# Performance work log

Hardware: AMD Instinct MI355X
Metric: run time of the kernel (lower is better)

## Reference

```python
import jax, jax.numpy as jnp
import numpy as np

NEG_INF = -(2.0**32) + 1.0  # matches tf: -2**32 + 1


def _positional_encoding(seq_len, d_model):
    # sinusoidal PE exactly as in the module (sin on even cols, cos on odd cols)
    pos = np.arange(seq_len)[:, None].astype(np.float32)
    i = np.arange(d_model)[None, :]
    angle_rates = 1.0 / np.power(10000.0, 2 * (i // 2) / np.float32(d_model))
    ang = pos * angle_rates
    ang[:, 0::2] = np.sin(ang[:, 0::2])
    ang[:, 1::2] = np.cos(ang[:, 1::2])
    return jnp.asarray(ang[None, ...], dtype=jnp.float32)  # [1, S, D]


def setup_inputs() -> dict:
    key = jax.random.key(0)
    kq, kk, kv, kw, km = jax.random.split(key, 5)
    B, S, D = 64, 512, 256
    q = jax.random.normal(kq, (B, S, D), dtype=jnp.float32)
    k = jax.random.normal(kk, (B, S, D), dtype=jnp.float32)
    v = jax.random.normal(kv, (B, S, D), dtype=jnp.float32)
    # keras 'random_uniform' initializer default range is [-0.05, 0.05]
    W = jax.random.uniform(kw, (D, D), dtype=jnp.float32, minval=-0.05, maxval=0.05)
    mask = jax.random.randint(km, (B, S), 0, 2, dtype=jnp.int32)
    return {"q": q, "k": k, "v": v, "W": W, "mask": mask}


def reference(q, k, v, W, mask):
    B, S, D = q.shape
    pe = _positional_encoding(S, D)  # [1, S, D]
    q = q + pe
    k = k + pe
    q = jax.nn.relu(jnp.einsum('bsd,de->bse', q, W))
    k = jax.nn.relu(jnp.einsum('bsd,de->bse', k, W))
    logits = jnp.einsum('bqd,bkd->bqk', q, k) / jnp.sqrt(jnp.float32(D))  # [B,S,S]
    # mask over key positions, broadcast across query dim
    logits = jnp.where(mask[:, None, :] == 0, jnp.float32(NEG_INF), logits)
    att = jax.nn.softmax(logits, axis=-1)
    out = jnp.einsum('bqk,bkd->bqd', att, v)
    return jnp.mean(out, axis=1)  # [B, D]
```

## Files before the change

kernel.cpp:

```cpp
#include <hip/hip_runtime.h>

#define NEG_INF (-4294967295.0f)

typedef _Float16 f16;
typedef _Float16 f16x8 __attribute__((ext_vector_type(8)));
typedef float f32x4 __attribute__((ext_vector_type(4)));

#define MFMA16(a,b,c) __builtin_amdgcn_mfma_f32_16x16x32_f16((a),(b),(c),0,0,0)

#if defined(__has_builtin)
#if __has_builtin(__builtin_amdgcn_global_load_lds)
#define HAS_GLD 1
#endif
#endif

__device__ __forceinline__ void stage16(const void* g, void* lds_base, int lane) {
#ifdef HAS_GLD
    __builtin_amdgcn_global_load_lds(
        (const __attribute__((address_space(1))) unsigned int*)g,
        (__attribute__((address_space(3))) unsigned int*)lds_base, 16, 0, 0);
#else
    ((f16x8*)lds_base)[lane] = *(const f16x8*)g;
#endif
}

__global__ __launch_bounds__(256) void setup_kernel(const float* __restrict__ W,
                                                    float* __restrict__ pe,
                                                    f16* __restrict__ WT,
                                                    float* __restrict__ WG,
                                                    float* __restrict__ out) {
    const int bid = blockIdx.x, t = threadIdx.x;
    if (bid < 512) {
        int idx = bid * 256 + t;
        int s = idx >> 8, d = idx & 255;
        float x = (float)(d & ~1) * (1.f / 256.f);
        float rate = exp2f(x * -13.287712379549449f);
        float ang = (float)s * rate;
        pe[idx] = (d & 1) ? cosf(ang) : sinf(ang);
    } else if (bid < 768) {
        int e = bid - 512, d = t;
        WT[(e << 8) + d] = (f16)W[(d << 8) + e];
    } else if (bid == 768) {
        #pragma unroll
        for (int i = 0; i < 128; ++i) WG[i * 256 + t] = 0.f;
    } else {
        #pragma unroll
        for (int i = 0; i < 64; ++i) out[i * 256 + t] = 0.f;
    }
}

__global__ __launch_bounds__(256, 4) void proj_kernel(const float* __restrict__ q,
                                                      const float* __restrict__ k,
                                                      const f16* __restrict__ WT,
                                                      const float* __restrict__ pe,
                                                      f16* __restrict__ outp) {
    __shared__ __align__(16) f16 Ws[256 * 64];
    const int t = threadIdx.x, l = t & 63, wv = t >> 6, lr = l & 15, lg = l >> 4;
    const int r0 = blockIdx.x * 64;
    const float* src = (r0 < 32768) ? q : k;
    const int rb = r0 & 32767;

    const float* arow = src + (size_t)(rb + wv * 16 + lr) * 256;
    const float* prow = pe + (size_t)((rb + wv * 16 + lr) & 511) * 256;
    f16x8 af[8];
    #pragma unroll
    for (int kk = 0; kk < 8; ++kk) {
        int d = kk * 32 + lg * 8;
        float4 a0 = *(const float4*)(arow + d);
        float4 a1 = *(const float4*)(arow + d + 4);
        float4 p0 = *(const float4*)(prow + d);
        float4 p1 = *(const float4*)(prow + d + 4);
        f16x8 h;
        h[0] = (f16)(a0.x + p0.x); h[1] = (f16)(a0.y + p0.y);
        h[2] = (f16)(a0.z + p0.z); h[3] = (f16)(a0.w + p0.w);
        h[4] = (f16)(a1.x + p1.x); h[5] = (f16)(a1.y + p1.y);
        h[6] = (f16)(a1.z + p1.z); h[7] = (f16)(a1.w + p1.w);
        af[kk] = h;
    }

    f32x4 acc[16] = {};
    #pragma unroll
    for (int kc = 0; kc < 4; ++kc) {
        #pragma unroll
        for (int it = 0; it < 8; ++it) {
            int eb = wv * 64 + it * 8;
            int e = eb + (l >> 3), c = l & 7;
            const f16* s = WT + (e << 8) + kc * 64 + ((c ^ (e & 7)) << 3);
            stage16(s, &Ws[eb << 6], l);
        }
        __syncthreads();
        #pragma unroll
        for (int kk = 0; kk < 2; ++kk) {
            int dk = kk * 32 + lg * 8;
            f16x8 a = af[kc * 2 + kk];
            #pragma unroll
            for (int nt = 0; nt < 16; ++nt) {
                int e = nt * 16 + lr;
                f16x8 b = *(const f16x8*)&Ws[(e << 6) + (dk ^ ((lr & 7) << 3))];
                acc[nt] = MFMA16(a, b, acc[nt]);
            }
        }
        __syncthreads();
    }

    f16* Rb = Ws + wv * 4096;
    #pragma unroll
    for (int nt = 0; nt < 16; ++nt) {
        #pragma unroll
        for (int rg = 0; rg < 4; ++rg) {
            int rr = lg * 4 + rg, col = nt * 16 + lr;
            float v = acc[nt][rg];
            v = v > 0.f ? v * 0.25f : 0.f;
            Rb[rr * 256 + ((((col >> 3) ^ (rr & 7)) << 3) | (col & 7))] = (f16)v;
        }
    }
    #pragma unroll
    for (int it = 0; it < 8; ++it) {
        int row = it * 2 + (l >> 5), c = l & 31;
        f16x8 v8 = *(const f16x8*)&Rb[row * 256 + ((c ^ (row & 7)) << 3)];
        *(f16x8*)(outp + (((size_t)(r0 + wv * 16 + row)) << 8) + c * 8) = v8;
    }
}

__global__ __launch_bounds__(256) void attn_kernel(const f16* __restrict__ QP,
                                                   const f16* __restrict__ KP,
                                                   const int* __restrict__ mask,
                                                   float* __restrict__ wglob) {
    __shared__ __align__(16) f16 Ks[2][32 * 256];
    __shared__ float ws[4][512];
    const int t = threadIdx.x, l = t & 63, wv = t >> 6, lr = l & 15, lg = l >> 4;
    const int n = blockIdx.x, bb = n & 63, qt = n >> 6;
    const int q0 = qt * 64 + wv * 16;
    const int* maskb = mask + bb * 512;

    auto stageK = [&](int dst, int kt) {
        #pragma unroll
        for (int it = 0; it < 4; ++it) {
            int r2 = wv * 8 + it * 2;
            int r = r2 + (l >> 5), c = l & 31;
            const f16* s = KP + (((size_t)(bb * 512 + kt * 32 + r)) << 8) + ((c ^ (r & 7)) << 3);
            stage16(s, &Ks[dst][r2 << 8], l);
        }
    };

    f16x8 qf[8];
    const f16* qrow = QP + (((size_t)(bb * 512 + q0 + lr)) << 8);
    #pragma unroll
    for (int kk = 0; kk < 8; ++kk) qf[kk] = *(const f16x8*)(qrow + kk * 32 + lg * 8);

    unsigned mb0 = 0, mb1 = 0;
    #pragma unroll
    for (int kt = 0; kt < 16; ++kt) {
        mb0 |= (maskb[kt * 32 + lr] ? 1u : 0u) << kt;
        mb1 |= (maskb[kt * 32 + 16 + lr] ? 1u : 0u) << kt;
    }

    float lacc[4] = {0.f, 0.f, 0.f, 0.f};
    f16 Pst[16][8];

    stageK(0, 0);
    __syncthreads();

    #pragma unroll
    for (int kt = 0; kt < 16; ++kt) {
        const int cur = kt & 1;
        if (kt < 15) stageK(cur ^ 1, kt + 1);
        f32x4 s0 = {}, s1 = {};
        #pragma unroll
        for (int kk = 0; kk < 8; ++kk) {
            int dk = kk * 32 + lg * 8;
            f16x8 b0 = *(const f16x8*)&Ks[cur][(lr << 8) + (dk ^ ((lr & 7) << 3))];
            f16x8 b1 = *(const f16x8*)&Ks[cur][((16 + lr) << 8) + (dk ^ ((lr & 7) << 3))];
            s0 = MFMA16(qf[kk], b0, s0);
            s1 = MFMA16(qf[kk], b1, s1);
        }
        #pragma unroll
        for (int rg = 0; rg < 4; ++rg) {
            float p0 = __expf(((mb0 >> kt) & 1) ? s0[rg] : NEG_INF);
            float p1 = __expf(((mb1 >> kt) & 1) ? s1[rg] : NEG_INF);
            f16 h0 = (f16)p0, h1 = (f16)p1;
            Pst[kt][rg] = h0;
            Pst[kt][4 + rg] = h1;
            lacc[rg] += (float)h0 + (float)h1;
        }
        if (kt < 15) __syncthreads();
    }

    #pragma unroll
    for (int rg = 0; rg < 4; ++rg) {
        float s = lacc[rg];
        s += __shfl_xor(s, 1); s += __shfl_xor(s, 2);
        s += __shfl_xor(s, 4); s += __shfl_xor(s, 8);
        lacc[rg] = s;
    }
    float rl[4];
    float bsum = 0.f;
    #pragma unroll
    for (int rg = 0; rg < 4; ++rg) {
        if (lacc[rg] > 0.f) { rl[rg] = 1.0f / lacc[rg]; }
        else                { rl[rg] = 0.f; bsum += 1.f / 512.f; }
    }

    #pragma unroll
    for (int kt = 0; kt < 16; ++kt) {
        float w0 = (float)Pst[kt][0] * rl[0] + (float)Pst[kt][1] * rl[1]
                 + (float)Pst[kt][2] * rl[2] + (float)Pst[kt][3] * rl[3] + bsum;
        float w1 = (float)Pst[kt][4] * rl[0] + (float)Pst[kt][5] * rl[1]
                 + (float)Pst[kt][6] * rl[2] + (float)Pst[kt][7] * rl[3] + bsum;
        w0 += __shfl_xor(w0, 16); w0 += __shfl_xor(w0, 32);
        w1 += __shfl_xor(w1, 16); w1 += __shfl_xor(w1, 32);
        if (lg == 0) {
            ws[wv][kt * 32 + lr] = w0;
            ws[wv][kt * 32 + 16 + lr] = w1;
        }
    }
    __syncthreads();
    #pragma unroll
    for (int i = 0; i < 2; ++i) {
        int kk = t + i * 256;
        float s = ws[0][kk] + ws[1][kk] + ws[2][kk] + ws[3][kk];
        atomicAdd(&wglob[bb * 512 + kk], s);
    }
}

__global__ __launch_bounds__(256) void wv_kernel(const float* __restrict__ wglob,
                                                 const float* __restrict__ V,
                                                 float* __restrict__ out) {
    const int n = blockIdx.x, bb = n & 63, ks = n >> 6;
    const int d = threadIdx.x;
    const float* wr = wglob + bb * 512 + ks * 64;
    const float* vb = V + ((((size_t)bb) * 512 + ks * 64) << 8) + d;
    float acc = 0.f;
    #pragma unroll 8
    for (int kk = 0; kk < 64; ++kk) acc = fmaf(wr[kk], vb[(size_t)kk << 8], acc);
    atomicAdd(&out[bb * 256 + d], acc * (1.f / 512.f));
}

extern "C" void kernel_launch(void* const* d_in, const int* in_sizes, int n_in,
                              void* d_out, int out_size, void* d_ws, size_t ws_size,
                              hipStream_t stream) {
    const float* q  = (const float*)d_in[0];
    const float* k  = (const float*)d_in[1];
    const float* v  = (const float*)d_in[2];
    const float* W  = (const float*)d_in[3];
    const int* mask = (const int*)d_in[4];

    char* ws = (char*)d_ws;
    f16*   QP = (f16*)ws;
    f16*   KP = (f16*)(ws + 16777216);
    float* PE = (float*)(ws + 33554432);
    f16*   WT = (f16*)(ws + 34078720);
    float* WG = (float*)(ws + 34209792);

    setup_kernel<<<770, 256, 0, stream>>>(W, PE, WT, WG, (float*)d_out);
    proj_kernel<<<1024, 256, 0, stream>>>(q, k, WT, PE, QP);
    attn_kernel<<<512, 256, 0, stream>>>(QP, KP, mask, WG);
    wv_kernel<<<512, 256, 0, stream>>>(WG, v, (float*)d_out);
}
```

Before: 170.2 us.

## Precompute PE@W and pipeline projection with 1024-thread blocks and LDS staging

```diff
diff --git a/kernel.cpp b/kernel.cpp
--- a/kernel.cpp
+++ b/kernel.cpp
@@ -25,21 +25,29 @@
 }
 
 __global__ __launch_bounds__(256) void setup_kernel(const float* __restrict__ W,
-                                                    float* __restrict__ pe,
                                                     f16* __restrict__ WT,
+                                                    float* __restrict__ PEW,
                                                     float* __restrict__ WG,
                                                     float* __restrict__ out) {
     const int bid = blockIdx.x, t = threadIdx.x;
     if (bid < 512) {
-        int idx = bid * 256 + t;
-        int s = idx >> 8, d = idx & 255;
-        float x = (float)(d & ~1) * (1.f / 256.f);
-        float rate = exp2f(x * -13.287712379549449f);
-        float ang = (float)s * rate;
-        pe[idx] = (d & 1) ? cosf(ang) : sinf(ang);
+        __shared__ float pr[256];
+        const int s = bid;
+        {
+            int d = t;
+            float x = (float)(d & ~1) * (1.f / 256.f);
+            float rate = exp2f(x * -13.287712379549449f);
+            float ang = (float)s * rate;
+            pr[d] = (d & 1) ? cosf(ang) : sinf(ang);
+        }
+        __syncthreads();
+        float acc = 0.f;
+        #pragma unroll 8
+        for (int d = 0; d < 256; ++d) acc = fmaf(pr[d], W[d * 256 + t], acc);
+        PEW[s * 256 + t] = acc;
     } else if (bid < 768) {
-        int e = bid - 512, d = t;
-        WT[(e << 8) + d] = (f16)W[(d << 8) + e];
+        int e = bid - 512;
+        WT[(e << 8) + t] = (f16)W[(t << 8) + e];
     } else if (bid == 768) {
         #pragma unroll
         for (int i = 0; i < 128; ++i) WG[i * 256 + t] = 0.f;
@@ -49,76 +57,82 @@
     }
 }
 
-__global__ __launch_bounds__(256, 4) void proj_kernel(const float* __restrict__ q,
-                                                      const float* __restrict__ k,
-                                                      const f16* __restrict__ WT,
-                                                      const float* __restrict__ pe,
-                                                      f16* __restrict__ outp) {
-    __shared__ __align__(16) f16 Ws[256 * 64];
+__global__ __launch_bounds__(1024, 4) void proj_kernel(const float* __restrict__ q,
+                                                       const float* __restrict__ k,
+                                                       const f16* __restrict__ WT,
+                                                       const float* __restrict__ PEW,
+                                                       f16* __restrict__ outp) {
+    __shared__ __align__(16) char lds[49152];
     const int t = threadIdx.x, l = t & 63, wv = t >> 6, lr = l & 15, lg = l >> 4;
+    const int wr = wv >> 2, wc = wv & 3;
     const int r0 = blockIdx.x * 64;
     const float* src = (r0 < 32768) ? q : k;
     const int rb = r0 & 32767;
 
-    const float* arow = src + (size_t)(rb + wv * 16 + lr) * 256;
-    const float* prow = pe + (size_t)((rb + wv * 16 + lr) & 511) * 256;
-    f16x8 af[8];
-    #pragma unroll
-    for (int kk = 0; kk < 8; ++kk) {
-        int d = kk * 32 + lg * 8;
-        float4 a0 = *(const float4*)(arow + d);
-        float4 a1 = *(const float4*)(arow + d + 4);
-        float4 p0 = *(const float4*)(prow + d);
-        float4 p1 = *(const float4*)(prow + d + 4);
-        f16x8 h;
-        h[0] = (f16)(a0.x + p0.x); h[1] = (f16)(a0.y + p0.y);
-        h[2] = (f16)(a0.z + p0.z); h[3] = (f16)(a0.w + p0.w);
-        h[4] = (f16)(a1.x + p1.x); h[5] = (f16)(a1.y + p1.y);
-        h[6] = (f16)(a1.z + p1.z); h[7] = (f16)(a1.w + p1.w);
-        af[kk] = h;
-    }
-
-    f32x4 acc[16] = {};
-    #pragma unroll
-    for (int kc = 0; kc < 4; ++kc) {
-        #pragma unroll
-        for (int it = 0; it < 8; ++it) {
-            int eb = wv * 64 + it * 8;
-            int e = eb + (l >> 3), c = l & 7;
-            const f16* s = WT + (e << 8) + kc * 64 + ((c ^ (e & 7)) << 3);
-            stage16(s, &Ws[eb << 6], l);
-        }
-        __syncthreads();
-        #pragma unroll
-        for (int kk = 0; kk < 2; ++kk) {
-            int dk = kk * 32 + lg * 8;
-            f16x8 a = af[kc * 2 + kk];
+    auto stageA = [&](int buf, int kc) {
+        if (wv < 8) {
+            int row = wv * 8 + (l >> 3);
+            const float* s = src + (size_t)(rb + row) * 256 + kc * 32
+                           + (((l & 7) ^ (l >> 3)) << 2);
+            stage16(s, lds + buf * 8192 + wv * 1024, l);
+        } else {
+            int w8 = wv - 8;
             #pragma unroll
-            for (int nt = 0; nt < 16; ++nt) {
-                int e = nt * 16 + lr;
-                f16x8 b = *(const f16x8*)&Ws[(e << 6) + (dk ^ ((lr & 7) << 3))];
-                acc[nt] = MFMA16(a, b, acc[nt]);
+            for (int it = 0; it < 2; ++it) {
+                int eb = w8 * 32 + it * 16;
+                int e = eb + (l >> 2);
+                const f16* s = WT + (e << 8) + kc * 32
+                             + (((l & 3) ^ ((l >> 3) & 3)) << 3);
+                stage16(s, lds + 16384 + buf * 16384 + (w8 * 2 + it) * 1024, l);
             }
         }
-        __syncthreads();
-    }
-
-    f16* Rb = Ws + wv * 4096;
-    #pragma unroll
-    for (int nt = 0; nt < 16; ++nt) {
+    };
+
+    f32x4 acc[4] = {};
+    stageA(0, 0);
+    __syncthreads();
+
+    #pragma unroll
+    for (int kc = 0; kc < 8; ++kc) {
+        const int cur = kc & 1;
+        if (kc < 7) stageA(cur ^ 1, kc + 1);
+        const float* Ab = (const float*)(lds + cur * 8192);
+        const f16* Wb = (const f16*)(lds + 16384 + cur * 16384);
+        int row_l = wr * 16 + lr;
+        float4 fa = *(const float4*)&Ab[row_l * 32 + ((((lg * 2)     ) ^ (lr & 7)) << 2)];
+        float4 fb = *(const float4*)&Ab[row_l * 32 + ((((lg * 2) | 1 ) ^ (lr & 7)) << 2)];
+        f16x8 af;
+        af[0] = (f16)fa.x; af[1] = (f16)fa.y; af[2] = (f16)fa.z; af[3] = (f16)fa.w;
+        af[4] = (f16)fb.x; af[5] = (f16)fb.y; af[6] = (f16)fb.z; af[7] = (f16)fb.w;
+        #pragma unroll
+        for (int nt = 0; nt < 4; ++nt) {
+            int e = wc * 64 + nt * 16 + lr;
+            f16x8 bf = *(const f16x8*)&Wb[(e << 5) + ((lg ^ ((lr >> 1) & 3)) << 3)];
+            acc[nt] = MFMA16(af, bf, acc[nt]);
+        }
+        if (kc < 7) __syncthreads();
+    }
+    __syncthreads();
+
+    f16* arena = (f16*)lds;
+    #pragma unroll
+    for (int nt = 0; nt < 4; ++nt) {
         #pragma unroll
         for (int rg = 0; rg < 4; ++rg) {
-            int rr = lg * 4 + rg, col = nt * 16 + lr;
-            float v = acc[nt][rg];
+            int row = wr * 16 + lg * 4 + rg;
+            int col = wc * 64 + nt * 16 + lr;
+            float v = acc[nt][rg] + PEW[(size_t)((r0 + row) & 511) * 256 + col];
             v = v > 0.f ? v * 0.25f : 0.f;
-            Rb[rr * 256 + ((((col >> 3) ^ (rr & 7)) << 3) | (col & 7))] = (f16)v;
-        }
-    }
-    #pragma unroll
-    for (int it = 0; it < 8; ++it) {
-        int row = it * 2 + (l >> 5), c = l & 31;
-        f16x8 v8 = *(const f16x8*)&Rb[row * 256 + ((c ^ (row & 7)) << 3)];
-        *(f16x8*)(outp + (((size_t)(r0 + wv * 16 + row)) << 8) + c * 8) = v8;
+            arena[row * 256 + ((((col >> 3) ^ (row & 7)) << 3) | (col & 7))] = (f16)v;
+        }
+    }
+    __syncthreads();
+    #pragma unroll
+    for (int i = 0; i < 2; ++i) {
+        int idx = i * 1024 + t;
+        int row = idx >> 5, ch = idx & 31;
+        f16x8 v8 = *(const f16x8*)&arena[row * 256 + ((ch ^ (row & 7)) << 3)];
+        *(f16x8*)(outp + (size_t)(r0 + row) * 256 + ch * 8) = v8;
     }
 }
 
@@ -246,14 +260,14 @@
     const int* mask = (const int*)d_in[4];
 
     char* ws = (char*)d_ws;
-    f16*   QP = (f16*)ws;
-    f16*   KP = (f16*)(ws + 16777216);
-    float* PE = (float*)(ws + 33554432);
-    f16*   WT = (f16*)(ws + 34078720);
-    float* WG = (float*)(ws + 34209792);
-
-    setup_kernel<<<770, 256, 0, stream>>>(W, PE, WT, WG, (float*)d_out);
-    proj_kernel<<<1024, 256, 0, stream>>>(q, k, WT, PE, QP);
+    f16*   QP  = (f16*)ws;
+    f16*   KP  = (f16*)(ws + 16777216);
+    f16*   WT  = (f16*)(ws + 33554432);
+    float* PEW = (float*)(ws + 33685504);
+    float* WG  = (float*)(ws + 34209792);
+
+    setup_kernel<<<770, 256, 0, stream>>>(W, WT, PEW, WG, (float*)d_out);
+    proj_kernel<<<1024, 1024, 0, stream>>>(q, k, WT, PEW, QP);
     attn_kernel<<<512, 256, 0, stream>>>(QP, KP, mask, WG);
     wv_kernel<<<512, 256, 0, stream>>>(WG, v, (float*)d_out);
 }
```

After: 186.8 us. 1.1x slower.
